# Kernel optimization log

Measured on AMD Instinct MI355X. Metric: run time of the kernel, lower is better.

## Reference

```python
import jax, jax.numpy as jnp
import numpy as np

B, S, H, NSPANS, NCLS = 32, 4096, 1024, 16, 25
MAX_SPAN_LEN = 64


def setup_inputs() -> dict:
    key = jax.random.key(0)
    k_emb, k_w1, k_b1, k_w2, k_b2 = jax.random.split(key, 5)
    all_emb = jax.random.normal(k_emb, (B, S, H), dtype=jnp.float32)

    # Build span table with (0,0) padding after the first n_valid spans
    # (the torch code breaks on the first (0,0) row).
    rng = np.random.default_rng(0)
    starts = rng.integers(1, S - MAX_SPAN_LEN, size=(B, NSPANS))
    lengths = rng.integers(1, MAX_SPAN_LEN, size=(B, NSPANS))
    ends = starts + lengths
    spans = np.stack([starts, ends], axis=-1).astype(np.int32)  # [B,N,2]
    n_valid = rng.integers(1, NSPANS + 1, size=(B,))
    for i in range(B):
        spans[i, n_valid[i]:, :] = 0
    sp_token_positions = jnp.asarray(spans)

    sc1 = 1.0 / np.sqrt(H)
    W1 = jax.random.normal(k_w1, (H, H), dtype=jnp.float32) * sc1
    b1 = jax.random.normal(k_b1, (H,), dtype=jnp.float32) * 0.01
    W2 = jax.random.normal(k_w2, (H, NCLS), dtype=jnp.float32) * sc1
    b2 = jax.random.normal(k_b2, (NCLS,), dtype=jnp.float32) * 0.01
    return {"all_emb": all_emb, "sp_token_positions": sp_token_positions,
            "W1": W1, "b1": b1, "W2": W2, "b2": b2}


def _span_mean(all_emb, spans):
    # spans: [B, N, 2] int32. A span is valid only if it is non-(0,0) AND all
    # earlier spans in its row are valid (torch 'break' semantics).
    s0 = spans[..., 0]  # [B,N]
    s1 = spans[..., 1]
    nonzero = ((s0 != 0) | (s1 != 0)).astype(jnp.float32)
    valid = jnp.cumprod(nonzero, axis=1)  # [B,N]

    t = jnp.arange(all_emb.shape[1])  # [S]
    # in_span[b,n,t] = start <= t < end; overlapping spans count tokens twice,
    # exactly like the torch.cat-then-mean original.
    in_span = ((t[None, None, :] >= s0[..., None]) &
               (t[None, None, :] < s1[..., None])).astype(jnp.float32)
    weights = jnp.einsum('bnt,bn->bt', in_span, valid)  # [B,S] token counts
    total = jnp.sum(weights, axis=1, keepdims=True)     # [B,1]
    summed = jnp.einsum('bsh,bs->bh', all_emb, weights)  # [B,H]
    return summed / total


def reference(all_emb, sp_token_positions, W1, b1, W2, b2):
    pooled = _span_mean(all_emb, sp_token_positions)        # [B,H]
    h = jax.nn.relu(pooled @ W1 + b1)                       # fc1 + relu
    logits = h @ W2 + b2                                    # fc2
    return jax.nn.sigmoid(logits)                           # [B,25]
```

## Files before the change

kernel.cpp:

```cpp
#include <hip/hip_runtime.h>
#include <math.h>

#define B      32
#define S      4096
#define H      1024
#define NSPANS 16
#define NCLS   25

__global__ __launch_bounds__(256) void span_pool_kernel(
    const float* __restrict__ emb,
    const int*   __restrict__ spans,
    float*       __restrict__ pooled)
{
    const int n = blockIdx.x;
    const int b = blockIdx.y;

    __shared__ int   sh_s0, sh_s1, sh_valid;
    __shared__ float sh_scale;

    if (threadIdx.x < 64) {
        const int k = threadIdx.x;
        int a = 0, e = 0;
        if (k < NSPANS) {
            a = spans[(b * NSPANS + k) * 2 + 0];
            e = spans[(b * NSPANS + k) * 2 + 1];
        }
        unsigned long long nzmask = __ballot((a | e) != 0);
        const int nvalid = (int)__builtin_ctzll(~nzmask);

        int len = (k < nvalid) ? (e - a) : 0;
        #pragma unroll
        for (int off = 32; off > 0; off >>= 1)
            len += __shfl_down(len, off, 64);

        if (k == 0) {
            sh_scale = (len > 0) ? (1.0f / (float)len) : 0.0f;
            sh_valid = (n < nvalid);
        }
        if (k == n) { sh_s0 = a; sh_s1 = e; }
    }
    __syncthreads();

    if (!sh_valid) return;
    const int   s0    = sh_s0;
    const int   s1    = sh_s1;
    const float scale = sh_scale;

    const float4* base = (const float4*)(emb + (size_t)b * S * H) + threadIdx.x;

    float4 a0 = make_float4(0.f, 0.f, 0.f, 0.f);
    float4 a1 = make_float4(0.f, 0.f, 0.f, 0.f);
    float4 a2 = make_float4(0.f, 0.f, 0.f, 0.f);
    float4 a3 = make_float4(0.f, 0.f, 0.f, 0.f);

    int t = s0;
    for (; t + 4 <= s1; t += 4) {
        float4 v0 = base[(size_t)(t + 0) * (H / 4)];
        float4 v1 = base[(size_t)(t + 1) * (H / 4)];
        float4 v2 = base[(size_t)(t + 2) * (H / 4)];
        float4 v3 = base[(size_t)(t + 3) * (H / 4)];
        a0.x += v0.x; a0.y += v0.y; a0.z += v0.z; a0.w += v0.w;
        a1.x += v1.x; a1.y += v1.y; a1.z += v1.z; a1.w += v1.w;
        a2.x += v2.x; a2.y += v2.y; a2.z += v2.z; a2.w += v2.w;
        a3.x += v3.x; a3.y += v3.y; a3.z += v3.z; a3.w += v3.w;
    }
    for (; t < s1; ++t) {
        float4 v = base[(size_t)t * (H / 4)];
        a0.x += v.x; a0.y += v.y; a0.z += v.z; a0.w += v.w;
    }

    a0.x += a1.x + a2.x + a3.x;
    a0.y += a1.y + a2.y + a3.y;
    a0.z += a1.z + a2.z + a3.z;
    a0.w += a1.w + a2.w + a3.w;

    float* dst = pooled + (size_t)b * H + threadIdx.x * 4;
    atomicAdd(dst + 0, a0.x * scale);
    atomicAdd(dst + 1, a0.y * scale);
    atomicAdd(dst + 2, a0.z * scale);
    atomicAdd(dst + 3, a0.w * scale);
}

__global__ __launch_bounds__(256) void fc1_relu_kernel(
    const float* __restrict__ pooled,
    const float* __restrict__ W1,
    const float* __restrict__ b1,
    float*       __restrict__ hbuf)
{
    const int b    = blockIdx.x >> 4;
    const int jblk = (blockIdx.x & 15) << 6;
    const int lane = threadIdx.x & 63;
    const int quad = threadIdx.x >> 6;
    const int j    = jblk + lane;

    __shared__ float pool_s[H];
    ((float4*)pool_s)[threadIdx.x] =
        ((const float4*)(pooled + (size_t)b * H))[threadIdx.x];
    __syncthreads();

    const float* w = W1 + j;
    float acc = 0.0f;
    const int i0 = quad * (H / 4);
    #pragma unroll 8
    for (int i = i0; i < i0 + H / 4; ++i) {
        acc = fmaf(pool_s[i], w[(size_t)i * H], acc);
    }

    __shared__ float part[4][64];
    part[quad][lane] = acc;
    __syncthreads();

    if (threadIdx.x < 64) {
        float s = part[0][lane] + part[1][lane] + part[2][lane] + part[3][lane]
                + b1[jblk + lane];
        hbuf[(size_t)b * H + jblk + lane] = fmaxf(s, 0.0f);
    }
}

__global__ __launch_bounds__(256) void fc2_sigmoid_kernel(
    const float* __restrict__ hbuf,
    const float* __restrict__ W2,
    const float* __restrict__ b2,
    float*       __restrict__ out)
{
    const int c = blockIdx.x;
    const int b = blockIdx.y;

    const float* hrow = hbuf + (size_t)b * H;
    float partial = 0.0f;
    #pragma unroll
    for (int i = threadIdx.x; i < H; i += 256) {
        partial = fmaf(hrow[i], W2[(size_t)i * NCLS + c], partial);
    }

    #pragma unroll
    for (int off = 32; off > 0; off >>= 1)
        partial += __shfl_down(partial, off, 64);

    __shared__ float wsum[4];
    const int wave = threadIdx.x >> 6;
    const int lane = threadIdx.x & 63;
    if (lane == 0) wsum[wave] = partial;
    __syncthreads();

    if (threadIdx.x == 0) {
        float s = wsum[0] + wsum[1] + wsum[2] + wsum[3] + b2[c];
        out[(size_t)b * NCLS + c] = 1.0f / (1.0f + expf(-s));
    }
}

extern "C" void kernel_launch(void* const* d_in, const int* in_sizes, int n_in,
                              void* d_out, int out_size, void* d_ws, size_t ws_size,
                              hipStream_t stream) {
    const float* emb   = (const float*)d_in[0];
    const int*   spans = (const int*)  d_in[1];
    const float* W1    = (const float*)d_in[2];
    const float* b1    = (const float*)d_in[3];
    const float* W2    = (const float*)d_in[4];
    const float* b2    = (const float*)d_in[5];
    float*       out   = (float*)d_out;

    float* pooled = (float*)d_ws;
    float* hbuf   = pooled + B * H;

    hipMemsetAsync(d_ws, 0, (size_t)B * H * sizeof(float), stream);

    span_pool_kernel<<<dim3(NSPANS, B), 256, 0, stream>>>(emb, spans, pooled);
    fc1_relu_kernel<<<dim3(B * 16), 256, 0, stream>>>(pooled, W1, b1, hbuf);
    fc2_sigmoid_kernel<<<dim3(NCLS, B), 256, 0, stream>>>(hbuf, W2, b2, out);
}
```

Before: 610.1 us.

## Replace atomic span pooling with per-span buffer; process two batches per fc1 block

The span kernel now writes each span's scaled partial sum to a dedicated per-span slot instead of atomically adding into pooled rows, which removes the memset and the float atomics. The fc1 kernel reduces the 16 span partials while loading into shared memory, and each block handles two batch rows so every W1 load is used twice, halving W1 traffic. The cost is extra workspace (B*NSPANS*H floats) and an extra read of that buffer in fc1.

Result: no change. 610.9 us (+0.1%).

```diff
diff --git a/kernel.cpp b/kernel.cpp
--- a/kernel.cpp
+++ b/kernel.cpp
@@ -10,7 +10,7 @@
 __global__ __launch_bounds__(256) void span_pool_kernel(
     const float* __restrict__ emb,
     const int*   __restrict__ spans,
-    float*       __restrict__ pooled)
+    float*       __restrict__ spanbuf)
 {
     const int n = blockIdx.x;
     const int b = blockIdx.y;
@@ -41,79 +41,105 @@
     }
     __syncthreads();
 
-    if (!sh_valid) return;
-    const int   s0    = sh_s0;
-    const int   s1    = sh_s1;
-    const float scale = sh_scale;
+    float4 r = make_float4(0.f, 0.f, 0.f, 0.f);
 
-    const float4* base = (const float4*)(emb + (size_t)b * S * H) + threadIdx.x;
+    if (sh_valid) {
+        const int   s0    = sh_s0;
+        const int   s1    = sh_s1;
+        const float scale = sh_scale;
 
-    float4 a0 = make_float4(0.f, 0.f, 0.f, 0.f);
-    float4 a1 = make_float4(0.f, 0.f, 0.f, 0.f);
-    float4 a2 = make_float4(0.f, 0.f, 0.f, 0.f);
-    float4 a3 = make_float4(0.f, 0.f, 0.f, 0.f);
+        const float4* base =
+            (const float4*)(emb + (size_t)b * S * H) + threadIdx.x;
 
-    int t = s0;
-    for (; t + 4 <= s1; t += 4) {
-        float4 v0 = base[(size_t)(t + 0) * (H / 4)];
-        float4 v1 = base[(size_t)(t + 1) * (H / 4)];
-        float4 v2 = base[(size_t)(t + 2) * (H / 4)];
-        float4 v3 = base[(size_t)(t + 3) * (H / 4)];
-        a0.x += v0.x; a0.y += v0.y; a0.z += v0.z; a0.w += v0.w;
-        a1.x += v1.x; a1.y += v1.y; a1.z += v1.z; a1.w += v1.w;
-        a2.x += v2.x; a2.y += v2.y; a2.z += v2.z; a2.w += v2.w;
-        a3.x += v3.x; a3.y += v3.y; a3.z += v3.z; a3.w += v3.w;
-    }
-    for (; t < s1; ++t) {
-        float4 v = base[(size_t)t * (H / 4)];
-        a0.x += v.x; a0.y += v.y; a0.z += v.z; a0.w += v.w;
+        float4 a0 = make_float4(0.f, 0.f, 0.f, 0.f);
+        float4 a1 = make_float4(0.f, 0.f, 0.f, 0.f);
+        float4 a2 = make_float4(0.f, 0.f, 0.f, 0.f);
+        float4 a3 = make_float4(0.f, 0.f, 0.f, 0.f);
+
+        int t = s0;
+        for (; t + 4 <= s1; t += 4) {
+            float4 v0 = base[(size_t)(t + 0) * (H / 4)];
+            float4 v1 = base[(size_t)(t + 1) * (H / 4)];
+            float4 v2 = base[(size_t)(t + 2) * (H / 4)];
+            float4 v3 = base[(size_t)(t + 3) * (H / 4)];
+            a0.x += v0.x; a0.y += v0.y; a0.z += v0.z; a0.w += v0.w;
+            a1.x += v1.x; a1.y += v1.y; a1.z += v1.z; a1.w += v1.w;
+            a2.x += v2.x; a2.y += v2.y; a2.z += v2.z; a2.w += v2.w;
+            a3.x += v3.x; a3.y += v3.y; a3.z += v3.z; a3.w += v3.w;
+        }
+        for (; t < s1; ++t) {
+            float4 v = base[(size_t)t * (H / 4)];
+            a0.x += v.x; a0.y += v.y; a0.z += v.z; a0.w += v.w;
+        }
+
+        r.x = (a0.x + a1.x + a2.x + a3.x) * scale;
+        r.y = (a0.y + a1.y + a2.y + a3.y) * scale;
+        r.z = (a0.z + a1.z + a2.z + a3.z) * scale;
+        r.w = (a0.w + a1.w + a2.w + a3.w) * scale;
     }
 
-    a0.x += a1.x + a2.x + a3.x;
-    a0.y += a1.y + a2.y + a3.y;
-    a0.z += a1.z + a2.z + a3.z;
-    a0.w += a1.w + a2.w + a3.w;
-
-    float* dst = pooled + (size_t)b * H + threadIdx.x * 4;
-    atomicAdd(dst + 0, a0.x * scale);
-    atomicAdd(dst + 1, a0.y * scale);
-    atomicAdd(dst + 2, a0.z * scale);
-    atomicAdd(dst + 3, a0.w * scale);
+    float4* dst = (float4*)(spanbuf + ((size_t)b * NSPANS + n) * H);
+    dst[threadIdx.x] = r;
 }
 
 __global__ __launch_bounds__(256) void fc1_relu_kernel(
-    const float* __restrict__ pooled,
+    const float* __restrict__ spanbuf,
     const float* __restrict__ W1,
     const float* __restrict__ b1,
     float*       __restrict__ hbuf)
 {
-    const int b    = blockIdx.x >> 4;
+    const int bp   = blockIdx.x >> 4;
     const int jblk = (blockIdx.x & 15) << 6;
+    const int b0   = bp * 2;
+    const int bb1  = bp * 2 + 1;
+
+    __shared__ float pool0[H];
+    __shared__ float pool1[H];
+
+    {
+        const float4* s0 =
+            (const float4*)(spanbuf + (size_t)b0 * NSPANS * H) + threadIdx.x;
+        const float4* s1 =
+            (const float4*)(spanbuf + (size_t)bb1 * NSPANS * H) + threadIdx.x;
+        float4 acc0 = make_float4(0.f, 0.f, 0.f, 0.f);
+        float4 acc1 = make_float4(0.f, 0.f, 0.f, 0.f);
+        #pragma unroll
+        for (int nn = 0; nn < NSPANS; ++nn) {
+            float4 v0 = s0[nn * (H / 4)];
+            float4 v1 = s1[nn * (H / 4)];
+            acc0.x += v0.x; acc0.y += v0.y; acc0.z += v0.z; acc0.w += v0.w;
+            acc1.x += v1.x; acc1.y += v1.y; acc1.z += v1.z; acc1.w += v1.w;
+        }
+        ((float4*)pool0)[threadIdx.x] = acc0;
+        ((float4*)pool1)[threadIdx.x] = acc1;
+    }
+    __syncthreads();
+
     const int lane = threadIdx.x & 63;
     const int quad = threadIdx.x >> 6;
     const int j    = jblk + lane;
 
-    __shared__ float pool_s[H];
-    ((float4*)pool_s)[threadIdx.x] =
-        ((const float4*)(pooled + (size_t)b * H))[threadIdx.x];
-    __syncthreads();
-
     const float* w = W1 + j;
-    float acc = 0.0f;
+    float a0 = 0.0f, a1 = 0.0f;
     const int i0 = quad * (H / 4);
     #pragma unroll 8
     for (int i = i0; i < i0 + H / 4; ++i) {
-        acc = fmaf(pool_s[i], w[(size_t)i * H], acc);
+        const float wv = w[(size_t)i * H];
+        a0 = fmaf(pool0[i], wv, a0);
+        a1 = fmaf(pool1[i], wv, a1);
     }
 
-    __shared__ float part[4][64];
-    part[quad][lane] = acc;
+    __shared__ float part[2][4][64];
+    part[0][quad][lane] = a0;
+    part[1][quad][lane] = a1;
     __syncthreads();
 
-    if (threadIdx.x < 64) {
-        float s = part[0][lane] + part[1][lane] + part[2][lane] + part[3][lane]
-                + b1[jblk + lane];
-        hbuf[(size_t)b * H + jblk + lane] = fmaxf(s, 0.0f);
+    if (threadIdx.x < 128) {
+        const int bb = threadIdx.x >> 6;
+        const int l  = threadIdx.x & 63;
+        float s = part[bb][0][l] + part[bb][1][l]
+                + part[bb][2][l] + part[bb][3][l] + b1[jblk + l];
+        hbuf[(size_t)(b0 + bb) * H + jblk + l] = fmaxf(s, 0.0f);
     }
 }
 
@@ -160,12 +186,11 @@
     const float* b2    = (const float*)d_in[5];
     float*       out   = (float*)d_out;
 
-    float* pooled = (float*)d_ws;
-    float* hbuf   = pooled + B * H;
+    float* spanbuf = (float*)d_ws;
+    float* hbuf    = spanbuf + (size_t)B * NSPANS * H;
 
-    hipMemsetAsync(d_ws, 0, (size_t)B * H * sizeof(float), stream);
 
-    span_pool_kernel<<<dim3(NSPANS, B), 256, 0, stream>>>(emb, spans, pooled);
-    fc1_relu_kernel<<<dim3(B * 16), 256, 0, stream>>>(pooled, W1, b1, hbuf);
+    span_pool_kernel<<<dim3(NSPANS, B), 256, 0, stream>>>(emb, spans, spanbuf);
+    fc1_relu_kernel<<<dim3(256), 256, 0, stream>>>(spanbuf, W1, b1, hbuf);
     fc2_sigmoid_kernel<<<dim3(NCLS, B), 256, 0, stream>>>(hbuf, W2, b2, out);
 }
```
